# Performance work log

Measured on AMD Instinct MI355X. Metric: run time of the kernel, lower is better.

Reference implementation:

```python
import jax, jax.numpy as jnp
import numpy as np

TEMP = 5.0      # torch_kmeans SoftKMeans default temperature
N_ITERS = 25    # fixed iteration count (tolerance-based stop removed for jit)
EPS = 1e-9


def _soft_kmeans(x, l, key):
    # x: (r, q, d) -> labels (r, q) int32, centers (r, l, d)
    r, q, d = x.shape
    keys = jax.random.split(key, r)
    # random-point init (one permutation per batch, first l points)
    idx = jax.vmap(lambda k: jax.random.permutation(k, q)[:l])(keys)  # (r, l)
    centers = jnp.take_along_axis(x, idx[:, :, None], axis=1)         # (r, l, d)
    x_sq = jnp.sum(x * x, axis=-1)                                    # (r, q)

    def dist_to(centers):
        # squared euclidean distance (r, q, l)
        return (x_sq[:, :, None]
                - 2.0 * jnp.einsum('rqd,rld->rql', x, centers)
                + jnp.sum(centers * centers, axis=-1)[:, None, :])

    def step(centers, _):
        w = jax.nn.softmax(-TEMP * dist_to(centers), axis=-1)         # (r, q, l)
        denom = jnp.sum(w, axis=1)[:, :, None] + EPS                  # (r, l, 1)
        centers = jnp.einsum('rql,rqd->rld', w, x) / denom
        return centers, None

    centers, _ = jax.lax.scan(step, centers, None, length=N_ITERS)
    labels = jnp.argmin(dist_to(centers), axis=-1)                    # (r, q)
    return labels, centers


def setup_inputs() -> dict:
    key = jax.random.key(0)
    x = jax.random.normal(key, (8, 2048, 1024), dtype=jnp.float32)
    return {"x": x, "q": 4096, "r": 8, "l": 256}


def reference(x, q, r, l):
    B, T, F = x.shape
    # B*T*F must equal r*q*d; mirrors x.view(B,-1).view(B,q,-1).view(r,q,-1)
    xr = x.reshape(r, q, -1)
    labels, centers = _soft_kmeans(xr, l, jax.random.key(42))
    # gather centroid per point: rec[b, i, :] = centers[b, labels[b, i], :]
    rec = jnp.take_along_axis(centers, labels[:, :, None], axis=1)    # (r, q, d)
    return rec.reshape(B, T, F)
```

## Files before the change

kernel.cpp:

```cpp
#include <hip/hip_runtime.h>
#include <stdint.h>

#define RB 8
#define QN 4096
#define DN 512
#define LN 256
#define NITERS 25

typedef double f64x4 __attribute__((ext_vector_type(4)));

__device__ __forceinline__ void tf2x32(uint32_t k0, uint32_t k1,
                                       uint32_t x0, uint32_t x1,
                                       uint32_t& y0, uint32_t& y1) {
  uint32_t ks2 = k0 ^ k1 ^ 0x1BD11BDAu;
#define TFR(r) { x0 += x1; x1 = (x1 << (r)) | (x1 >> (32 - (r))); x1 ^= x0; }
  x0 += k0; x1 += k1;
  TFR(13) TFR(15) TFR(26) TFR(6)   x0 += k1;  x1 += ks2 + 1u;
  TFR(17) TFR(29) TFR(16) TFR(24)  x0 += ks2; x1 += k0 + 2u;
  TFR(13) TFR(15) TFR(26) TFR(6)   x0 += k0;  x1 += k1 + 3u;
  TFR(17) TFR(29) TFR(16) TFR(24)  x0 += k1;  x1 += ks2 + 4u;
  TFR(13) TFR(15) TFR(26) TFR(6)   x0 += ks2; x1 += k0 + 5u;
#undef TFR
  y0 = x0; y1 = x1;
}

__global__ __launch_bounds__(1024) void k_init(const float* __restrict__ x,
                                               float* __restrict__ centers) {
  __shared__ unsigned long long comp[QN];
  __shared__ unsigned short perm[QN];
  __shared__ unsigned short ptmp[QN];
  const int b = blockIdx.x, t = threadIdx.x;

  uint32_t kb0, kb1;
  tf2x32(0u, 42u, 0u, (uint32_t)b, kb0, kb1);

  for (int i = t; i < QN; i += 1024) perm[i] = (unsigned short)i;
  __syncthreads();

  for (int round = 0; round < 2; ++round) {
    uint32_t nk0, nk1, sk0, sk1;
    tf2x32(kb0, kb1, 0u, 0u, nk0, nk1);
    tf2x32(kb0, kb1, 0u, 1u, sk0, sk1);
    kb0 = nk0; kb1 = nk1;
    for (int i = t; i < QN; i += 1024) {
      uint32_t y0, y1;
      tf2x32(sk0, sk1, 0u, (uint32_t)i, y0, y1);
      uint32_t bits = y0 ^ y1;
      comp[i] = ((unsigned long long)bits << 32) | (unsigned)i;
    }
    __syncthreads();
    for (int k = 2; k <= QN; k <<= 1) {
      for (int j = k >> 1; j > 0; j >>= 1) {
        for (int i = t; i < QN; i += 1024) {
          int ixj = i ^ j;
          if (ixj > i) {
            unsigned long long vi = comp[i], vj = comp[ixj];
            bool up = ((i & k) == 0);
            bool sw = up ? (vi > vj) : (vi < vj);
            if (sw) { comp[i] = vj; comp[ixj] = vi; }
          }
        }
        __syncthreads();
      }
    }
    for (int i = t; i < QN; i += 1024) ptmp[i] = perm[(unsigned)(comp[i] & 0xFFFFu)];
    __syncthreads();
    for (int i = t; i < QN; i += 1024) perm[i] = ptmp[i];
    __syncthreads();
  }

  const float4* xb = (const float4*)(x + (size_t)b * QN * DN);
  float4* cb = (float4*)(centers + (size_t)b * LN * DN);
  for (int e = t; e < LN * (DN / 4); e += 1024) {
    int row = e >> 7;
    int c = e & 127;
    cb[(size_t)row * 128 + c] = xb[(size_t)perm[row] * 128 + c];
  }
}

__global__ __launch_bounds__(256) void k_rowsq_d(const float* __restrict__ a,
                                                 double* __restrict__ o, int nrows) {
  int w = (blockIdx.x * 256 + threadIdx.x) >> 6;
  int lane = threadIdx.x & 63;
  if (w >= nrows) return;
  const float* row = a + (size_t)w * DN;
  double s = 0.0;
  for (int i = lane; i < DN; i += 64) { double v = (double)row[i]; s = fma(v, v, s); }
#pragma unroll
  for (int off = 32; off; off >>= 1) s += __shfl_down(s, off);
  if (lane == 0) o[w] = s;
}

__global__ __launch_bounds__(64) void k_probe(int* __restrict__ flag) {
  __shared__ double xT[16][17];
  __shared__ double cT[16][17];
  const int t = threadIdx.x;
  for (int i = t; i < 256; i += 64) {
    int r = i >> 4, d = i & 15;
    xT[d][r] = (double)(r * 5 + d * 3 + 1);
    cT[d][r] = (double)(r * 2 + d * 7 + 2);
  }
  __syncthreads();
  const int kg = t >> 4, li = t & 15;
  f64x4 acc = {0.0, 0.0, 0.0, 0.0};
#pragma unroll
  for (int kk = 0; kk < 4; kk++) {
    double a  = xT[kk * 4 + kg][li];
    double bv = cT[kk * 4 + kg][li];
    acc = __builtin_amdgcn_mfma_f64_16x16x4f64(a, bv, acc, 0, 0, 0);
  }
  bool ok1 = true, ok2 = true;
#pragma unroll
  for (int d = 0; d < 4; d++) {
    int q1 = kg * 4 + d;
    int q2 = kg + 4 * d;
    double ref1 = 0.0, ref2 = 0.0;
    for (int dd = 0; dd < 16; dd++) {
      ref1 += xT[dd][q1] * cT[dd][li];
      ref2 += xT[dd][q2] * cT[dd][li];
    }
    ok1 = ok1 && (acc[d] == ref1);
    ok2 = ok2 && (acc[d] == ref2);
  }
  unsigned long long v1 = __ballot(ok1);
  unsigned long long v2 = __ballot(ok2);
  if (t == 0) *flag = (v1 == ~0ull) ? 1 : ((v2 == ~0ull) ? 2 : 0);
}

#define QT 64
#define XPD 68
#define CPD 260

__global__ __launch_bounds__(256, 2) void k_assign_mfma(const float* __restrict__ x,
                                                        const float* __restrict__ centers,
                                                        const double* __restrict__ csqd,
                                                        float* __restrict__ W,
                                                        const int* __restrict__ flag) {
  const int mode = *flag;
  if (mode == 0) return;
  __shared__ double xT[16][XPD];
  __shared__ double cT[16][CPD];
  const int b = blockIdx.y, q0 = blockIdx.x * QT, t = threadIdx.x;
  const int w = t >> 6, lane = t & 63;
  const int kg = lane >> 4, li = lane & 15;

  f64x4 acc[16];
#pragma unroll
  for (int i = 0; i < 16; i++) acc[i] = (f64x4){0.0, 0.0, 0.0, 0.0};

  const float* xb = x + ((size_t)b * QN + q0) * DN;
  const float* cb = centers + (size_t)b * LN * DN;
  const int xrow = t >> 2, xc4 = t & 3;

  float4 gx, gc[4];
  gx = *(const float4*)(xb + (size_t)xrow * DN + xc4 * 4);
#pragma unroll
  for (int i = 0; i < 4; i++) {
    int f = t + 256 * i; int row = f >> 2, c4 = f & 3;
    gc[i] = *(const float4*)(cb + (size_t)row * DN + c4 * 4);
  }

  for (int d0 = 0; d0 < DN; d0 += 16) {
    xT[xc4 * 4 + 0][xrow] = (double)gx.x;
    xT[xc4 * 4 + 1][xrow] = (double)gx.y;
    xT[xc4 * 4 + 2][xrow] = (double)gx.z;
    xT[xc4 * 4 + 3][xrow] = (double)gx.w;
#pragma unroll
    for (int i = 0; i < 4; i++) {
      int f = t + 256 * i; int row = f >> 2, c4 = f & 3;
      cT[c4 * 4 + 0][row] = (double)gc[i].x;
      cT[c4 * 4 + 1][row] = (double)gc[i].y;
      cT[c4 * 4 + 2][row] = (double)gc[i].z;
      cT[c4 * 4 + 3][row] = (double)gc[i].w;
    }
    __syncthreads();
    if (d0 + 16 < DN) {
      gx = *(const float4*)(xb + (size_t)xrow * DN + (d0 + 16) + xc4 * 4);
#pragma unroll
      for (int i = 0; i < 4; i++) {
        int f = t + 256 * i; int row = f >> 2, c4 = f & 3;
        gc[i] = *(const float4*)(cb + (size_t)row * DN + (d0 + 16) + c4 * 4);
      }
    }
#pragma unroll
    for (int kk = 0; kk < 4; kk++) {
      double a = xT[kk * 4 + kg][w * 16 + li];
#pragma unroll
      for (int t16 = 0; t16 < 16; t16++) {
        double bv = cT[kk * 4 + kg][t16 * 16 + li];
        acc[t16] = __builtin_amdgcn_mfma_f64_16x16x4f64(a, bv, acc[t16], 0, 0, 0);
      }
    }
    __syncthreads();
  }

  double m[4] = {-1e300, -1e300, -1e300, -1e300};
#pragma unroll
  for (int t16 = 0; t16 < 16; t16++) {
    double cq = csqd[b * LN + t16 * 16 + li];
#pragma unroll
    for (int d = 0; d < 4; d++) {
      double lg = -5.0 * (cq - 2.0 * acc[t16][d]);
      acc[t16][d] = lg;
      m[d] = fmax(m[d], lg);
    }
  }
#pragma unroll
  for (int off = 1; off < 16; off <<= 1)
#pragma unroll
    for (int d = 0; d < 4; d++) m[d] = fmax(m[d], __shfl_xor(m[d], off, 64));

  double s[4] = {0.0, 0.0, 0.0, 0.0};
#pragma unroll
  for (int t16 = 0; t16 < 16; t16++)
#pragma unroll
    for (int d = 0; d < 4; d++) {
      double e = exp(acc[t16][d] - m[d]);
      acc[t16][d] = e;
      s[d] += e;
    }
#pragma unroll
  for (int off = 1; off < 16; off <<= 1)
#pragma unroll
    for (int d = 0; d < 4; d++) s[d] += __shfl_xor(s[d], off, 64);

  const size_t qbase = (size_t)b * QN + q0 + w * 16;
#pragma unroll
  for (int d = 0; d < 4; d++) {
    int qrow = (mode == 1) ? (kg * 4 + d) : (kg + 4 * d);
    float* wrow = W + (qbase + qrow) * LN + li;
    double inv = 1.0 / s[d];
#pragma unroll
    for (int t16 = 0; t16 < 16; t16++)
      wrow[t16 * 16] = (float)(acc[t16][d] * inv);
  }
}

#define DK 16
#define XLD 82
#define CLDf 260
__device__ __forceinline__ int grow(int q) { return q + ((q >> 3) << 1); }

__global__ __launch_bounds__(256, 2) void k_assign_valu(const float* __restrict__ x,
                                                        const float* __restrict__ centers,
                                                        const double* __restrict__ csqd,
                                                        float* __restrict__ W,
                                                        const int* __restrict__ flag) {
  if (*flag != 0) return;
  __shared__ double xsD[DK][XLD];
  __shared__ float  csF[DK][CLDf];
  __shared__ double red[QT][33];
  const int b = blockIdx.y, q0 = blockIdx.x * QT, t = threadIdx.x;
  const int rg = t & 7, cg = t >> 3;
  double acc[8][8];
#pragma unroll
  for (int i = 0; i < 8; i++)
#pragma unroll
    for (int j = 0; j < 8; j++) acc[i][j] = 0.0;

  const float* xb = x + ((size_t)b * QN + q0) * DN;
  const float* cb = centers + (size_t)b * LN * DN;
  const int xrow = t >> 2, xc4 = t & 3;
  const int xg = grow(xrow);

  float4 gx, gc[4];
  gx = *(const float4*)(xb + (size_t)xrow * DN + xc4 * 4);
#pragma unroll
  for (int i = 0; i < 4; i++) {
    int f = t + 256 * i; int row = f >> 2, c4 = f & 3;
    gc[i] = *(const float4*)(cb + (size_t)row * DN + c4 * 4);
  }

  for (int d0 = 0; d0 < DN; d0 += DK) {
    xsD[xc4 * 4 + 0][xg] = (double)gx.x; xsD[xc4 * 4 + 1][xg] = (double)gx.y;
    xsD[xc4 * 4 + 2][xg] = (double)gx.z; xsD[xc4 * 4 + 3][xg] = (double)gx.w;
#pragma unroll
    for (int i = 0; i < 4; i++) {
      int f = t + 256 * i; int row = f >> 2, c4 = f & 3;
      csF[c4 * 4 + 0][row] = gc[i].x; csF[c4 * 4 + 1][row] = gc[i].y;
      csF[c4 * 4 + 2][row] = gc[i].z; csF[c4 * 4 + 3][row] = gc[i].w;
    }
    __syncthreads();
    if (d0 + DK < DN) {
      gx = *(const float4*)(xb + (size_t)xrow * DN + (d0 + DK) + xc4 * 4);
#pragma unroll
      for (int i = 0; i < 4; i++) {
        int f = t + 256 * i; int row = f >> 2, c4 = f & 3;
        gc[i] = *(const float4*)(cb + (size_t)row * DN + (d0 + DK) + c4 * 4);
      }
    }
    double xva[8]; float4 ca0, ca1;
#pragma unroll
    for (int j = 0; j < 8; j++) xva[j] = xsD[0][rg * 10 + j];
    ca0 = *(const float4*)&csF[0][cg * 8];
    ca1 = *(const float4*)&csF[0][cg * 8 + 4];
#pragma unroll
    for (int k = 0; k < DK; k++) {
      double xvb[8]; float4 cb0, cb1;
      if (k + 1 < DK) {
#pragma unroll
        for (int j = 0; j < 8; j++) xvb[j] = xsD[k + 1][rg * 10 + j];
        cb0 = *(const float4*)&csF[k + 1][cg * 8];
        cb1 = *(const float4*)&csF[k + 1][cg * 8 + 4];
      }
      double cv[8] = {(double)ca0.x, (double)ca0.y, (double)ca0.z, (double)ca0.w,
                      (double)ca1.x, (double)ca1.y, (double)ca1.z, (double)ca1.w};
#pragma unroll
      for (int i = 0; i < 8; i++)
#pragma unroll
        for (int j = 0; j < 8; j++)
          acc[i][j] = fma(xva[i], cv[j], acc[i][j]);
      if (k + 1 < DK) {
#pragma unroll
        for (int j = 0; j < 8; j++) xva[j] = xvb[j];
        ca0 = cb0; ca1 = cb1;
      }
    }
    __syncthreads();
  }

  double csqv[8];
#pragma unroll
  for (int j = 0; j < 8; j++) csqv[j] = csqd[b * LN + cg * 8 + j];

  double lmax[8];
#pragma unroll
  for (int i = 0; i < 8; i++) {
    double m = -1e300;
#pragma unroll
    for (int j = 0; j < 8; j++) {
      double lg = -5.0 * (csqv[j] - 2.0 * acc[i][j]);
      acc[i][j] = lg;
      m = fmax(m, lg);
    }
    lmax[i] = m;
  }
#pragma unroll
  for (int i = 0; i < 8; i++) red[rg * 8 + i][cg] = lmax[i];
  __syncthreads();
  double rmax[8];
#pragma unroll
  for (int i = 0; i < 8; i++) {
    double m = -1e300;
    for (int c = 0; c < 32; c++) m = fmax(m, red[rg * 8 + i][c]);
    rmax[i] = m;
  }
  __syncthreads();
#pragma unroll
  for (int i = 0; i < 8; i++) {
    double s = 0.0;
#pragma unroll
    for (int j = 0; j < 8; j++) {
      double e = exp(acc[i][j] - rmax[i]);
      acc[i][j] = e;
      s += e;
    }
    red[rg * 8 + i][cg] = s;
  }
  __syncthreads();
#pragma unroll
  for (int i = 0; i < 8; i++) {
    double s = 0.0;
    for (int c = 0; c < 32; c++) s += red[rg * 8 + i][c];
    float* wrow = W + ((size_t)b * QN + q0 + rg * 8 + i) * LN + cg * 8;
    float4 v0 = make_float4((float)(acc[i][0] / s), (float)(acc[i][1] / s),
                            (float)(acc[i][2] / s), (float)(acc[i][3] / s));
    float4 v1 = make_float4((float)(acc[i][4] / s), (float)(acc[i][5] / s),
                            (float)(acc[i][6] / s), (float)(acc[i][7] / s));
    *(float4*)wrow = v0;
    *(float4*)(wrow + 4) = v1;
  }
}

#define NCH 8
#define CHQ (QN / NCH)
#define UKQ 16

__global__ __launch_bounds__(256, 3) void k_update_split(
    const float* __restrict__ W, const float* __restrict__ x,
    float* __restrict__ P, float* __restrict__ dsum) {
  __shared__ float wT[UKQ][132];
  __shared__ float xT[UKQ][132];
  const int b = blockIdx.z;
  const int s = blockIdx.y;
  const int lt = (blockIdx.x >> 2) * 128;
  const int dt = (blockIdx.x & 3) * 128;
  const int t = threadIdx.x;
  const int tr = t >> 4, tc = t & 15;
  float acc[8][8];
#pragma unroll
  for (int i = 0; i < 8; i++)
#pragma unroll
    for (int j = 0; j < 8; j++) acc[i][j] = 0.f;
  float dsm[8] = {0, 0, 0, 0, 0, 0, 0, 0};

  const float* Wb = W + ((size_t)b * QN + (size_t)s * CHQ) * LN + lt;
  const float* xb = x + ((size_t)b * QN + (size_t)s * CHQ) * DN + dt;

  float4 gw[2], gx2[2];
#pragma unroll
  for (int i = 0; i < 2; i++) {
    int f = t + 256 * i; int row = f >> 5, c = f & 31;
    gw[i]  = *(const float4*)(Wb + (size_t)row * LN + c * 4);
    gx2[i] = *(const float4*)(xb + (size_t)row * DN + c * 4);
  }

  for (int k0 = 0; k0 < CHQ; k0 += UKQ) {
#pragma unroll
    for (int i = 0; i < 2; i++) {
      int f = t + 256 * i; int row = f >> 5, c = f & 31;
      *(float4*)&wT[row][c * 4] = gw[i];
      *(float4*)&xT[row][c * 4] = gx2[i];
    }
    __syncthreads();
    if (k0 + UKQ < CHQ) {
#pragma unroll
      for (int i = 0; i < 2; i++) {
        int f = t + 256 * i; int row = f >> 5, c = f & 31;
        gw[i]  = *(const float4*)(Wb + (size_t)(k0 + UKQ + row) * LN + c * 4);
        gx2[i] = *(const float4*)(xb + (size_t)(k0 + UKQ + row) * DN + c * 4);
      }
    }
#pragma unroll
    for (int k = 0; k < UKQ; k++) {
      float4 w0 = *(const float4*)&wT[k][tr * 4];
      float4 w1 = *(const float4*)&wT[k][64 + tr * 4];
      float4 x0 = *(const float4*)&xT[k][tc * 4];
      float4 x1 = *(const float4*)&xT[k][64 + tc * 4];
      float wf[8] = {w0.x, w0.y, w0.z, w0.w, w1.x, w1.y, w1.z, w1.w};
      float xf[8] = {x0.x, x0.y, x0.z, x0.w, x1.x, x1.y, x1.z, x1.w};
#pragma unroll
      for (int i = 0; i < 8; i++) {
        dsm[i] += wf[i];
#pragma unroll
        for (int j = 0; j < 8; j++) acc[i][j] = fmaf(wf[i], xf[j], acc[i][j]);
      }
    }
    __syncthreads();
  }

#pragma unroll
  for (int i = 0; i < 8; i++) {
    int l = lt + ((i < 4) ? (tr * 4 + i) : (64 + tr * 4 + i - 4));
    float* prow = P + (((size_t)s * RB + b) * LN + l) * DN + dt;
    *(float4*)(prow + tc * 4)      = make_float4(acc[i][0], acc[i][1], acc[i][2], acc[i][3]);
    *(float4*)(prow + 64 + tc * 4) = make_float4(acc[i][4], acc[i][5], acc[i][6], acc[i][7]);
    if (tc == 0) dsum[((size_t)s * RB + b) * LN + l] = dsm[i];
  }
}

__global__ __launch_bounds__(128) void k_reduce(const float* __restrict__ P,
                                                const float* __restrict__ dsum,
                                                float* __restrict__ cnew,
                                                double* __restrict__ csqd) {
  const int row = blockIdx.x;
  const int b = row >> 8, l = row & 255;
  const int t = threadIdx.x;
  float dn = 0.f;
#pragma unroll
  for (int s = 0; s < NCH; s++) dn += dsum[((size_t)s * RB + b) * LN + l];
  float den = dn + 1e-9f;
  float4 v = make_float4(0.f, 0.f, 0.f, 0.f);
#pragma unroll
  for (int s = 0; s < NCH; s++) {
    float4 p = *(const float4*)(P + (((size_t)s * RB + b) * LN + l) * DN + t * 4);
    v.x += p.x; v.y += p.y; v.z += p.z; v.w += p.w;
  }
  float4 o = make_float4(v.x / den, v.y / den, v.z / den, v.w / den);
  *(float4*)(cnew + ((size_t)b * LN + l) * DN + t * 4) = o;
  double sq = (double)o.x * o.x + (double)o.y * o.y +
              (double)o.z * o.z + (double)o.w * o.w;
#pragma unroll
  for (int off = 32; off; off >>= 1) sq += __shfl_down(sq, off);
  __shared__ double sred[2];
  if ((t & 63) == 0) sred[t >> 6] = sq;
  __syncthreads();
  if (t == 0) csqd[row] = sred[0] + sred[1];
}

#define LT 64
#define DT 64
#define KQ 32
__global__ __launch_bounds__(256) void k_update_mono(const float* __restrict__ W,
                                                     const float* __restrict__ x,
                                                     float* __restrict__ cnew) {
  __shared__ float wT[KQ][LT + 4];
  __shared__ float xT[KQ][DT + 4];
  const int b = blockIdx.z;
  const int l0 = blockIdx.x * LT;
  const int d0 = blockIdx.y * DT;
  const int t = threadIdx.x;
  const int rg = t & 15;
  const int cg = t >> 4;
  float acc[4][4];
#pragma unroll
  for (int i = 0; i < 4; i++)
#pragma unroll
    for (int j = 0; j < 4; j++) acc[i][j] = 0.f;
  float dsm[4] = {0.f, 0.f, 0.f, 0.f};
  const float* Wb = W + (size_t)b * QN * LN;
  const float* xb = x + (size_t)b * QN * DN;
  for (int k0 = 0; k0 < QN; k0 += KQ) {
#pragma unroll
    for (int i = 0; i < 2; i++) {
      int f = t + 256 * i;
      int row = f >> 4, c4 = f & 15;
      *(float4*)&wT[row][c4 * 4] = *(const float4*)(Wb + (size_t)(k0 + row) * LN + l0 + c4 * 4);
    }
#pragma unroll
    for (int i = 0; i < 2; i++) {
      int f = t + 256 * i;
      int row = f >> 4, c4 = f & 15;
      *(float4*)&xT[row][c4 * 4] = *(const float4*)(xb + (size_t)(k0 + row) * DN + d0 + c4 * 4);
    }
    __syncthreads();
#pragma unroll
    for (int k = 0; k < KQ; k++) {
      float wf[4], xf[4];
      *(float4*)wf = *(const float4*)&wT[k][rg * 4];
      *(float4*)xf = *(const float4*)&xT[k][cg * 4];
#pragma unroll
      for (int i = 0; i < 4; i++) {
        dsm[i] += wf[i];
#pragma unroll
        for (int j = 0; j < 4; j++) acc[i][j] = fmaf(wf[i], xf[j], acc[i][j]);
      }
    }
    __syncthreads();
  }
#pragma unroll
  for (int i = 0; i < 4; i++) {
    float den = dsm[i] + 1e-9f;
    *(float4*)(cnew + ((size_t)b * LN + l0 + rg * 4 + i) * DN + d0 + cg * 4) =
        make_float4(acc[i][0] / den, acc[i][1] / den, acc[i][2] / den, acc[i][3] / den);
  }
}

__global__ __launch_bounds__(256, 2) void k_final(const float* __restrict__ x,
                                                  const float* __restrict__ centers,
                                                  const double* __restrict__ csqd,
                                                  float* __restrict__ out) {
  __shared__ double xsD[DK][XLD];
  __shared__ float  csF[DK][CLDf];
  __shared__ double redv[QT][33];
  __shared__ unsigned short redi[QT][33];
  __shared__ unsigned short labels[QT];
  const int b = blockIdx.y, q0 = blockIdx.x * QT, t = threadIdx.x;
  const int rg = t & 7, cg = t >> 3;
  double acc[8][8];
#pragma unroll
  for (int i = 0; i < 8; i++)
#pragma unroll
    for (int j = 0; j < 8; j++) acc[i][j] = 0.0;

  const float* xb = x + ((size_t)b * QN + q0) * DN;
  const float* cb = centers + (size_t)b * LN * DN;
  const int xrow = t >> 2, xc4 = t & 3;
  const int xg = grow(xrow);

  float4 gx, gc[4];
  gx = *(const float4*)(xb + (size_t)xrow * DN + xc4 * 4);
#pragma unroll
  for (int i = 0; i < 4; i++) {
    int f = t + 256 * i; int row = f >> 2, c4 = f & 3;
    gc[i] = *(const float4*)(cb + (size_t)row * DN + c4 * 4);
  }

  for (int d0 = 0; d0 < DN; d0 += DK) {
    xsD[xc4 * 4 + 0][xg] = (double)gx.x; xsD[xc4 * 4 + 1][xg] = (double)gx.y;
    xsD[xc4 * 4 + 2][xg] = (double)gx.z; xsD[xc4 * 4 + 3][xg] = (double)gx.w;
#pragma unroll
    for (int i = 0; i < 4; i++) {
      int f = t + 256 * i; int row = f >> 2, c4 = f & 3;
      csF[c4 * 4 + 0][row] = gc[i].x; csF[c4 * 4 + 1][row] = gc[i].y;
      csF[c4 * 4 + 2][row] = gc[i].z; csF[c4 * 4 + 3][row] = gc[i].w;
    }
    __syncthreads();
    if (d0 + DK < DN) {
      gx = *(const float4*)(xb + (size_t)xrow * DN + (d0 + DK) + xc4 * 4);
#pragma unroll
      for (int i = 0; i < 4; i++) {
        int f = t + 256 * i; int row = f >> 2, c4 = f & 3;
        gc[i] = *(const float4*)(cb + (size_t)row * DN + (d0 + DK) + c4 * 4);
      }
    }
    double xva[8]; float4 ca0, ca1;
#pragma unroll
    for (int j = 0; j < 8; j++) xva[j] = xsD[0][rg * 10 + j];
    ca0 = *(const float4*)&csF[0][cg * 8];
    ca1 = *(const float4*)&csF[0][cg * 8 + 4];
#pragma unroll
    for (int k = 0; k < DK; k++) {
      double xvb[8]; float4 cb0, cb1;
      if (k + 1 < DK) {
#pragma unroll
        for (int j = 0; j < 8; j++) xvb[j] = xsD[k + 1][rg * 10 + j];
        cb0 = *(const float4*)&csF[k + 1][cg * 8];
        cb1 = *(const float4*)&csF[k + 1][cg * 8 + 4];
      }
      double cv[8] = {(double)ca0.x, (double)ca0.y, (double)ca0.z, (double)ca0.w,
                      (double)ca1.x, (double)ca1.y, (double)ca1.z, (double)ca1.w};
#pragma unroll
      for (int i = 0; i < 8; i++)
#pragma unroll
        for (int j = 0; j < 8; j++)
          acc[i][j] = fma(xva[i], cv[j], acc[i][j]);
      if (k + 1 < DK) {
#pragma unroll
        for (int j = 0; j < 8; j++) xva[j] = xvb[j];
        ca0 = cb0; ca1 = cb1;
      }
    }
    __syncthreads();
  }

  double csqv[8];
#pragma unroll
  for (int j = 0; j < 8; j++) csqv[j] = csqd[b * LN + cg * 8 + j];

  double bv[8]; int bi[8];
#pragma unroll
  for (int i = 0; i < 8; i++) {
    bv[i] = 1e300; bi[i] = 0;
#pragma unroll
    for (int j = 0; j < 8; j++) {
      double dd = csqv[j] - 2.0 * acc[i][j];
      if (dd < bv[i]) { bv[i] = dd; bi[i] = cg * 8 + j; }
    }
  }
#pragma unroll
  for (int i = 0; i < 8; i++) {
    redv[rg * 8 + i][cg] = bv[i];
    redi[rg * 8 + i][cg] = (unsigned short)bi[i];
  }
  __syncthreads();
  if (t < QT) {
    double best = 1e300; int bidx = 0;
    for (int c = 0; c < 32; c++) {
      double v = redv[t][c];
      int id = redi[t][c];
      if (v < best || (v == best && id < bidx)) { best = v; bidx = id; }
    }
    labels[t] = (unsigned short)bidx;
  }
  __syncthreads();
  const float4* cb4 = (const float4*)(centers + (size_t)b * LN * DN);
  float4* ob = (float4*)(out + ((size_t)b * QN + q0) * DN);
  for (int e = t; e < QT * (DN / 4); e += 256) {
    int row = e >> 7, c = e & 127;
    ob[(size_t)row * 128 + c] = cb4[(size_t)labels[row] * 128 + c];
  }
}

extern "C" void kernel_launch(void* const* d_in, const int* in_sizes, int n_in,
                              void* d_out, int out_size, void* d_ws, size_t ws_size,
                              hipStream_t stream) {
  const float* x = (const float*)d_in[0];
  float* out = (float*)d_out;

  const size_t szC    = (size_t)RB * LN * DN * sizeof(float);
  const size_t szCsqD = (size_t)RB * LN * sizeof(double);
  const size_t szDsum = (size_t)NCH * RB * LN * sizeof(float);
  const size_t szFlag = 256;
  const size_t szW    = (size_t)RB * QN * LN * sizeof(float);

  char* p = (char*)d_ws;
  float*  cA   = (float*)p;  p += szC;
  float*  cB   = (float*)p;  p += szC;
  double* csqd = (double*)p; p += szCsqD;
  float*  dsum = (float*)p;  p += szDsum;
  int*    flag = (int*)p;    p += szFlag;
  const bool bigws = ws_size >= 2 * szC + szCsqD + szDsum + szFlag + szW;
  float* W = bigws ? (float*)p : (float*)d_out;
  float* P = (float*)d_out;

  k_probe<<<1, 64, 0, stream>>>(flag);
  k_init<<<RB, 1024, 0, stream>>>(x, cA);
  k_rowsq_d<<<(RB * LN) / 4, 256, 0, stream>>>(cA, csqd, RB * LN);

  float* cur = cA;
  float* nxt = cB;
  for (int it = 0; it < NITERS; ++it) {
    k_assign_mfma<<<dim3(QN / QT, RB), 256, 0, stream>>>(x, cur, csqd, W, flag);
    k_assign_valu<<<dim3(QN / QT, RB), 256, 0, stream>>>(x, cur, csqd, W, flag);
    if (bigws) {
      k_update_split<<<dim3(8, NCH, RB), 256, 0, stream>>>(W, x, P, dsum);
      k_reduce<<<RB * LN, 128, 0, stream>>>(P, dsum, nxt, csqd);
    } else {
      k_update_mono<<<dim3(LN / LT, DN / DT, RB), 256, 0, stream>>>(W, x, nxt);
      k_rowsq_d<<<(RB * LN) / 4, 256, 0, stream>>>(nxt, csqd, RB * LN);
    }
    float* tmp = cur; cur = nxt; nxt = tmp;
  }
  k_final<<<dim3(QN / QT, RB), 256, 0, stream>>>(x, cur, csqd, out);
}
```

Measured before the change: 7.803 ms.

## Merge assign kernels and retile FP64 MFMA as 4x4 tiles per wave

The separate MFMA and VALU assignment kernels become one kernel that branches on the probe flag, so each iteration launches one kernel instead of two. The MFMA path is retiled: each wave now owns a 64-query by 64-center block built from 4x4 MFMA tiles, reusing four A and four B fragments across 16 MFMAs instead of reloading B for every MFMA. Because a wave now covers only part of the centers, the softmax max and sum need a cross-wave reduction through shared memory, which adds two extra barriers. Both paths share one shared-memory arena sized for the larger of the two.

Measured after the change: 8.011 ms. 2.7% more time.

```diff
diff --git a/kernel.cpp b/kernel.cpp
--- a/kernel.cpp
+++ b/kernel.cpp
@@ -130,245 +130,287 @@
 #define QT 64
 #define XPD 68
 #define CPD 260
-
-__global__ __launch_bounds__(256, 2) void k_assign_mfma(const float* __restrict__ x,
-                                                        const float* __restrict__ centers,
-                                                        const double* __restrict__ csqd,
-                                                        float* __restrict__ W,
-                                                        const int* __restrict__ flag) {
-  const int mode = *flag;
-  if (mode == 0) return;
-  __shared__ double xT[16][XPD];
-  __shared__ double cT[16][CPD];
-  const int b = blockIdx.y, q0 = blockIdx.x * QT, t = threadIdx.x;
-  const int w = t >> 6, lane = t & 63;
-  const int kg = lane >> 4, li = lane & 15;
-
-  f64x4 acc[16];
-#pragma unroll
-  for (int i = 0; i < 16; i++) acc[i] = (f64x4){0.0, 0.0, 0.0, 0.0};
-
-  const float* xb = x + ((size_t)b * QN + q0) * DN;
-  const float* cb = centers + (size_t)b * LN * DN;
-  const int xrow = t >> 2, xc4 = t & 3;
-
-  float4 gx, gc[4];
-  gx = *(const float4*)(xb + (size_t)xrow * DN + xc4 * 4);
-#pragma unroll
-  for (int i = 0; i < 4; i++) {
-    int f = t + 256 * i; int row = f >> 2, c4 = f & 3;
-    gc[i] = *(const float4*)(cb + (size_t)row * DN + c4 * 4);
-  }
-
-  for (int d0 = 0; d0 < DN; d0 += 16) {
-    xT[xc4 * 4 + 0][xrow] = (double)gx.x;
-    xT[xc4 * 4 + 1][xrow] = (double)gx.y;
-    xT[xc4 * 4 + 2][xrow] = (double)gx.z;
-    xT[xc4 * 4 + 3][xrow] = (double)gx.w;
-#pragma unroll
-    for (int i = 0; i < 4; i++) {
-      int f = t + 256 * i; int row = f >> 2, c4 = f & 3;
-      cT[c4 * 4 + 0][row] = (double)gc[i].x;
-      cT[c4 * 4 + 1][row] = (double)gc[i].y;
-      cT[c4 * 4 + 2][row] = (double)gc[i].z;
-      cT[c4 * 4 + 3][row] = (double)gc[i].w;
-    }
-    __syncthreads();
-    if (d0 + 16 < DN) {
-      gx = *(const float4*)(xb + (size_t)xrow * DN + (d0 + 16) + xc4 * 4);
-#pragma unroll
-      for (int i = 0; i < 4; i++) {
-        int f = t + 256 * i; int row = f >> 2, c4 = f & 3;
-        gc[i] = *(const float4*)(cb + (size_t)row * DN + (d0 + 16) + c4 * 4);
-      }
-    }
-#pragma unroll
-    for (int kk = 0; kk < 4; kk++) {
-      double a = xT[kk * 4 + kg][w * 16 + li];
-#pragma unroll
-      for (int t16 = 0; t16 < 16; t16++) {
-        double bv = cT[kk * 4 + kg][t16 * 16 + li];
-        acc[t16] = __builtin_amdgcn_mfma_f64_16x16x4f64(a, bv, acc[t16], 0, 0, 0);
-      }
-    }
-    __syncthreads();
-  }
-
-  double m[4] = {-1e300, -1e300, -1e300, -1e300};
-#pragma unroll
-  for (int t16 = 0; t16 < 16; t16++) {
-    double cq = csqd[b * LN + t16 * 16 + li];
-#pragma unroll
-    for (int d = 0; d < 4; d++) {
-      double lg = -5.0 * (cq - 2.0 * acc[t16][d]);
-      acc[t16][d] = lg;
-      m[d] = fmax(m[d], lg);
-    }
-  }
-#pragma unroll
-  for (int off = 1; off < 16; off <<= 1)
-#pragma unroll
-    for (int d = 0; d < 4; d++) m[d] = fmax(m[d], __shfl_xor(m[d], off, 64));
-
-  double s[4] = {0.0, 0.0, 0.0, 0.0};
-#pragma unroll
-  for (int t16 = 0; t16 < 16; t16++)
-#pragma unroll
-    for (int d = 0; d < 4; d++) {
-      double e = exp(acc[t16][d] - m[d]);
-      acc[t16][d] = e;
-      s[d] += e;
-    }
-#pragma unroll
-  for (int off = 1; off < 16; off <<= 1)
-#pragma unroll
-    for (int d = 0; d < 4; d++) s[d] += __shfl_xor(s[d], off, 64);
-
-  const size_t qbase = (size_t)b * QN + q0 + w * 16;
-#pragma unroll
-  for (int d = 0; d < 4; d++) {
-    int qrow = (mode == 1) ? (kg * 4 + d) : (kg + 4 * d);
-    float* wrow = W + (qbase + qrow) * LN + li;
-    double inv = 1.0 / s[d];
-#pragma unroll
-    for (int t16 = 0; t16 < 16; t16++)
-      wrow[t16 * 16] = (float)(acc[t16][d] * inv);
-  }
-}
-
 #define DK 16
 #define XLD 82
 #define CLDf 260
 __device__ __forceinline__ int grow(int q) { return q + ((q >> 3) << 1); }
 
-__global__ __launch_bounds__(256, 2) void k_assign_valu(const float* __restrict__ x,
-                                                        const float* __restrict__ centers,
-                                                        const double* __restrict__ csqd,
-                                                        float* __restrict__ W,
-                                                        const int* __restrict__ flag) {
-  if (*flag != 0) return;
-  __shared__ double xsD[DK][XLD];
-  __shared__ float  csF[DK][CLDf];
-  __shared__ double red[QT][33];
+#define ARENA_D 5888
+
+__global__ __launch_bounds__(256, 2) void k_assign(const float* __restrict__ x,
+                                                   const float* __restrict__ centers,
+                                                   const double* __restrict__ csqd,
+                                                   float* __restrict__ W,
+                                                   const int* __restrict__ flag) {
+  __shared__ double arena[ARENA_D];
+  const int mode = *flag;
   const int b = blockIdx.y, q0 = blockIdx.x * QT, t = threadIdx.x;
-  const int rg = t & 7, cg = t >> 3;
-  double acc[8][8];
-#pragma unroll
-  for (int i = 0; i < 8; i++)
-#pragma unroll
-    for (int j = 0; j < 8; j++) acc[i][j] = 0.0;
-
   const float* xb = x + ((size_t)b * QN + q0) * DN;
   const float* cb = centers + (size_t)b * LN * DN;
   const int xrow = t >> 2, xc4 = t & 3;
-  const int xg = grow(xrow);
-
-  float4 gx, gc[4];
-  gx = *(const float4*)(xb + (size_t)xrow * DN + xc4 * 4);
-#pragma unroll
-  for (int i = 0; i < 4; i++) {
-    int f = t + 256 * i; int row = f >> 2, c4 = f & 3;
-    gc[i] = *(const float4*)(cb + (size_t)row * DN + c4 * 4);
-  }
-
-  for (int d0 = 0; d0 < DN; d0 += DK) {
-    xsD[xc4 * 4 + 0][xg] = (double)gx.x; xsD[xc4 * 4 + 1][xg] = (double)gx.y;
-    xsD[xc4 * 4 + 2][xg] = (double)gx.z; xsD[xc4 * 4 + 3][xg] = (double)gx.w;
+
+  if (mode != 0) {
+    double (*xT)[XPD]  = (double(*)[XPD])arena;
+    double (*cT)[CPD]  = (double(*)[CPD])(arena + 16 * XPD);
+    double (*redm)[5]  = (double(*)[5])(arena + 16 * XPD + 16 * CPD);
+    double (*reds)[5]  = (double(*)[5])(arena + 16 * XPD + 16 * CPD + 320);
+    const int w = t >> 6, lane = t & 63;
+    const int kg = lane >> 4, li = lane & 15;
+
+    f64x4 acc[4][4];
+#pragma unroll
+    for (int i = 0; i < 4; i++)
+#pragma unroll
+      for (int j = 0; j < 4; j++) acc[i][j] = (f64x4){0.0, 0.0, 0.0, 0.0};
+
+    float4 gx, gc[4];
+    gx = *(const float4*)(xb + (size_t)xrow * DN + xc4 * 4);
 #pragma unroll
     for (int i = 0; i < 4; i++) {
       int f = t + 256 * i; int row = f >> 2, c4 = f & 3;
-      csF[c4 * 4 + 0][row] = gc[i].x; csF[c4 * 4 + 1][row] = gc[i].y;
-      csF[c4 * 4 + 2][row] = gc[i].z; csF[c4 * 4 + 3][row] = gc[i].w;
-    }
-    __syncthreads();
-    if (d0 + DK < DN) {
-      gx = *(const float4*)(xb + (size_t)xrow * DN + (d0 + DK) + xc4 * 4);
+      gc[i] = *(const float4*)(cb + (size_t)row * DN + c4 * 4);
+    }
+
+    for (int d0 = 0; d0 < DN; d0 += 16) {
+      xT[xc4 * 4 + 0][xrow] = (double)gx.x;
+      xT[xc4 * 4 + 1][xrow] = (double)gx.y;
+      xT[xc4 * 4 + 2][xrow] = (double)gx.z;
+      xT[xc4 * 4 + 3][xrow] = (double)gx.w;
 #pragma unroll
       for (int i = 0; i < 4; i++) {
         int f = t + 256 * i; int row = f >> 2, c4 = f & 3;
-        gc[i] = *(const float4*)(cb + (size_t)row * DN + (d0 + DK) + c4 * 4);
-      }
-    }
-    double xva[8]; float4 ca0, ca1;
-#pragma unroll
-    for (int j = 0; j < 8; j++) xva[j] = xsD[0][rg * 10 + j];
-    ca0 = *(const float4*)&csF[0][cg * 8];
-    ca1 = *(const float4*)&csF[0][cg * 8 + 4];
-#pragma unroll
-    for (int k = 0; k < DK; k++) {
-      double xvb[8]; float4 cb0, cb1;
-      if (k + 1 < DK) {
-#pragma unroll
-        for (int j = 0; j < 8; j++) xvb[j] = xsD[k + 1][rg * 10 + j];
-        cb0 = *(const float4*)&csF[k + 1][cg * 8];
-        cb1 = *(const float4*)&csF[k + 1][cg * 8 + 4];
-      }
-      double cv[8] = {(double)ca0.x, (double)ca0.y, (double)ca0.z, (double)ca0.w,
-                      (double)ca1.x, (double)ca1.y, (double)ca1.z, (double)ca1.w};
-#pragma unroll
-      for (int i = 0; i < 8; i++)
-#pragma unroll
-        for (int j = 0; j < 8; j++)
-          acc[i][j] = fma(xva[i], cv[j], acc[i][j]);
-      if (k + 1 < DK) {
-#pragma unroll
-        for (int j = 0; j < 8; j++) xva[j] = xvb[j];
-        ca0 = cb0; ca1 = cb1;
-      }
-    }
-    __syncthreads();
-  }
-
-  double csqv[8];
-#pragma unroll
-  for (int j = 0; j < 8; j++) csqv[j] = csqd[b * LN + cg * 8 + j];
-
-  double lmax[8];
-#pragma unroll
-  for (int i = 0; i < 8; i++) {
-    double m = -1e300;
-#pragma unroll
-    for (int j = 0; j < 8; j++) {
-      double lg = -5.0 * (csqv[j] - 2.0 * acc[i][j]);
-      acc[i][j] = lg;
-      m = fmax(m, lg);
-    }
-    lmax[i] = m;
-  }
-#pragma unroll
-  for (int i = 0; i < 8; i++) red[rg * 8 + i][cg] = lmax[i];
-  __syncthreads();
-  double rmax[8];
-#pragma unroll
-  for (int i = 0; i < 8; i++) {
-    double m = -1e300;
-    for (int c = 0; c < 32; c++) m = fmax(m, red[rg * 8 + i][c]);
-    rmax[i] = m;
-  }
-  __syncthreads();
-#pragma unroll
-  for (int i = 0; i < 8; i++) {
-    double s = 0.0;
-#pragma unroll
-    for (int j = 0; j < 8; j++) {
-      double e = exp(acc[i][j] - rmax[i]);
-      acc[i][j] = e;
-      s += e;
-    }
-    red[rg * 8 + i][cg] = s;
-  }
-  __syncthreads();
-#pragma unroll
-  for (int i = 0; i < 8; i++) {
-    double s = 0.0;
-    for (int c = 0; c < 32; c++) s += red[rg * 8 + i][c];
-    float* wrow = W + ((size_t)b * QN + q0 + rg * 8 + i) * LN + cg * 8;
-    float4 v0 = make_float4((float)(acc[i][0] / s), (float)(acc[i][1] / s),
-                            (float)(acc[i][2] / s), (float)(acc[i][3] / s));
-    float4 v1 = make_float4((float)(acc[i][4] / s), (float)(acc[i][5] / s),
-                            (float)(acc[i][6] / s), (float)(acc[i][7] / s));
-    *(float4*)wrow = v0;
-    *(float4*)(wrow + 4) = v1;
+        cT[c4 * 4 + 0][row] = (double)gc[i].x;
+        cT[c4 * 4 + 1][row] = (double)gc[i].y;
+        cT[c4 * 4 + 2][row] = (double)gc[i].z;
+        cT[c4 * 4 + 3][row] = (double)gc[i].w;
+      }
+      __syncthreads();
+      if (d0 + 16 < DN) {
+        gx = *(const float4*)(xb + (size_t)xrow * DN + (d0 + 16) + xc4 * 4);
+#pragma unroll
+        for (int i = 0; i < 4; i++) {
+          int f = t + 256 * i; int row = f >> 2, c4 = f & 3;
+          gc[i] = *(const float4*)(cb + (size_t)row * DN + (d0 + 16) + c4 * 4);
+        }
+      }
+#pragma unroll
+      for (int kk = 0; kk < 4; kk++) {
+        double a[4], bf[4];
+#pragma unroll
+        for (int qt = 0; qt < 4; qt++) a[qt] = xT[kk * 4 + kg][qt * 16 + li];
+#pragma unroll
+        for (int lt = 0; lt < 4; lt++) bf[lt] = cT[kk * 4 + kg][w * 64 + lt * 16 + li];
+#pragma unroll
+        for (int qt = 0; qt < 4; qt++)
+#pragma unroll
+          for (int lt = 0; lt < 4; lt++)
+            acc[qt][lt] = __builtin_amdgcn_mfma_f64_16x16x4f64(a[qt], bf[lt], acc[qt][lt], 0, 0, 0);
+      }
+      __syncthreads();
+    }
+
+    double csqv[4];
+#pragma unroll
+    for (int lt = 0; lt < 4; lt++) csqv[lt] = csqd[b * LN + w * 64 + lt * 16 + li];
+
+    double rm[4][4];
+#pragma unroll
+    for (int qt = 0; qt < 4; qt++)
+#pragma unroll
+      for (int d = 0; d < 4; d++) {
+        double m = -1e300;
+#pragma unroll
+        for (int lt = 0; lt < 4; lt++) {
+          double lg = -5.0 * (csqv[lt] - 2.0 * acc[qt][lt][d]);
+          acc[qt][lt][d] = lg;
+          m = fmax(m, lg);
+        }
+        rm[qt][d] = m;
+      }
+#pragma unroll
+    for (int off = 1; off < 16; off <<= 1)
+#pragma unroll
+      for (int qt = 0; qt < 4; qt++)
+#pragma unroll
+        for (int d = 0; d < 4; d++) rm[qt][d] = fmax(rm[qt][d], __shfl_xor(rm[qt][d], off, 64));
+    if (li == 0) {
+#pragma unroll
+      for (int qt = 0; qt < 4; qt++)
+#pragma unroll
+        for (int d = 0; d < 4; d++) {
+          int qr = qt * 16 + ((mode == 1) ? (kg * 4 + d) : (kg + 4 * d));
+          redm[qr][w] = rm[qt][d];
+        }
+    }
+    __syncthreads();
+#pragma unroll
+    for (int qt = 0; qt < 4; qt++)
+#pragma unroll
+      for (int d = 0; d < 4; d++) {
+        int qr = qt * 16 + ((mode == 1) ? (kg * 4 + d) : (kg + 4 * d));
+        rm[qt][d] = fmax(fmax(redm[qr][0], redm[qr][1]), fmax(redm[qr][2], redm[qr][3]));
+      }
+    double sv[4][4];
+#pragma unroll
+    for (int qt = 0; qt < 4; qt++)
+#pragma unroll
+      for (int d = 0; d < 4; d++) {
+        double s = 0.0;
+#pragma unroll
+        for (int lt = 0; lt < 4; lt++) {
+          double e = exp(acc[qt][lt][d] - rm[qt][d]);
+          acc[qt][lt][d] = e;
+          s += e;
+        }
+        sv[qt][d] = s;
+      }
+#pragma unroll
+    for (int off = 1; off < 16; off <<= 1)
+#pragma unroll
+      for (int qt = 0; qt < 4; qt++)
+#pragma unroll
+        for (int d = 0; d < 4; d++) sv[qt][d] += __shfl_xor(sv[qt][d], off, 64);
+    if (li == 0) {
+#pragma unroll
+      for (int qt = 0; qt < 4; qt++)
+#pragma unroll
+        for (int d = 0; d < 4; d++) {
+          int qr = qt * 16 + ((mode == 1) ? (kg * 4 + d) : (kg + 4 * d));
+          reds[qr][w] = sv[qt][d];
+        }
+    }
+    __syncthreads();
+#pragma unroll
+    for (int qt = 0; qt < 4; qt++)
+#pragma unroll
+      for (int d = 0; d < 4; d++) {
+        int qr = qt * 16 + ((mode == 1) ? (kg * 4 + d) : (kg + 4 * d));
+        double tot = reds[qr][0] + reds[qr][1] + reds[qr][2] + reds[qr][3];
+        double inv = 1.0 / tot;
+        float* wr = W + ((size_t)b * QN + q0 + qr) * LN + w * 64 + li;
+#pragma unroll
+        for (int lt = 0; lt < 4; lt++)
+          wr[lt * 16] = (float)(acc[qt][lt][d] * inv);
+      }
+  } else {
+    double (*xsD)[XLD]  = (double(*)[XLD])arena;
+    float  (*csF)[CLDf] = (float(*)[CLDf])(arena + 16 * XLD);
+    double (*red)[33]   = (double(*)[33])(arena + 16 * XLD + (16 * CLDf) / 2);
+    const int rg = t & 7, cg = t >> 3;
+    double acc[8][8];
+#pragma unroll
+    for (int i = 0; i < 8; i++)
+#pragma unroll
+      for (int j = 0; j < 8; j++) acc[i][j] = 0.0;
+
+    const int xg = grow(xrow);
+    float4 gx, gc[4];
+    gx = *(const float4*)(xb + (size_t)xrow * DN + xc4 * 4);
+#pragma unroll
+    for (int i = 0; i < 4; i++) {
+      int f = t + 256 * i; int row = f >> 2, c4 = f & 3;
+      gc[i] = *(const float4*)(cb + (size_t)row * DN + c4 * 4);
+    }
+
+    for (int d0 = 0; d0 < DN; d0 += DK) {
+      xsD[xc4 * 4 + 0][xg] = (double)gx.x; xsD[xc4 * 4 + 1][xg] = (double)gx.y;
+      xsD[xc4 * 4 + 2][xg] = (double)gx.z; xsD[xc4 * 4 + 3][xg] = (double)gx.w;
+#pragma unroll
+      for (int i = 0; i < 4; i++) {
+        int f = t + 256 * i; int row = f >> 2, c4 = f & 3;
+        csF[c4 * 4 + 0][row] = gc[i].x; csF[c4 * 4 + 1][row] = gc[i].y;
+        csF[c4 * 4 + 2][row] = gc[i].z; csF[c4 * 4 + 3][row] = gc[i].w;
+      }
+      __syncthreads();
+      if (d0 + DK < DN) {
+        gx = *(const float4*)(xb + (size_t)xrow * DN + (d0 + DK) + xc4 * 4);
+#pragma unroll
+        for (int i = 0; i < 4; i++) {
+          int f = t + 256 * i; int row = f >> 2, c4 = f & 3;
+          gc[i] = *(const float4*)(cb + (size_t)row * DN + (d0 + DK) + c4 * 4);
+        }
+      }
+      double xva[8]; float4 ca0, ca1;
+#pragma unroll
+      for (int j = 0; j < 8; j++) xva[j] = xsD[0][rg * 10 + j];
+      ca0 = *(const float4*)&csF[0][cg * 8];
+      ca1 = *(const float4*)&csF[0][cg * 8 + 4];
+#pragma unroll
+      for (int k = 0; k < DK; k++) {
+        double xvb[8]; float4 cb0, cb1;
+        if (k + 1 < DK) {
+#pragma unroll
+          for (int j = 0; j < 8; j++) xvb[j] = xsD[k + 1][rg * 10 + j];
+          cb0 = *(const float4*)&csF[k + 1][cg * 8];
+          cb1 = *(const float4*)&csF[k + 1][cg * 8 + 4];
+        }
+        double cv[8] = {(double)ca0.x, (double)ca0.y, (double)ca0.z, (double)ca0.w,
+                        (double)ca1.x, (double)ca1.y, (double)ca1.z, (double)ca1.w};
+#pragma unroll
+        for (int i = 0; i < 8; i++)
+#pragma unroll
+          for (int j = 0; j < 8; j++)
+            acc[i][j] = fma(xva[i], cv[j], acc[i][j]);
+        if (k + 1 < DK) {
+#pragma unroll
+          for (int j = 0; j < 8; j++) xva[j] = xvb[j];
+          ca0 = cb0; ca1 = cb1;
+        }
+      }
+      __syncthreads();
+    }
+
+    double csqv[8];
+#pragma unroll
+    for (int j = 0; j < 8; j++) csqv[j] = csqd[b * LN + cg * 8 + j];
+
+    double lmax[8];
+#pragma unroll
+    for (int i = 0; i < 8; i++) {
+      double m = -1e300;
+#pragma unroll
+      for (int j = 0; j < 8; j++) {
+        double lg = -5.0 * (csqv[j] - 2.0 * acc[i][j]);
+        acc[i][j] = lg;
+        m = fmax(m, lg);
+      }
+      lmax[i] = m;
+    }
+#pragma unroll
+    for (int i = 0; i < 8; i++) red[rg * 8 + i][cg] = lmax[i];
+    __syncthreads();
+    double rmax[8];
+#pragma unroll
+    for (int i = 0; i < 8; i++) {
+      double m = -1e300;
+      for (int c = 0; c < 32; c++) m = fmax(m, red[rg * 8 + i][c]);
+      rmax[i] = m;
+    }
+    __syncthreads();
+#pragma unroll
+    for (int i = 0; i < 8; i++) {
+      double s = 0.0;
+#pragma unroll
+      for (int j = 0; j < 8; j++) {
+        double e = exp(acc[i][j] - rmax[i]);
+        acc[i][j] = e;
+        s += e;
+      }
+      red[rg * 8 + i][cg] = s;
+    }
+    __syncthreads();
+#pragma unroll
+    for (int i = 0; i < 8; i++) {
+      double s = 0.0;
+      for (int c = 0; c < 32; c++) s += red[rg * 8 + i][c];
+      float* wrow = W + ((size_t)b * QN + q0 + rg * 8 + i) * LN + cg * 8;
+      float4 v0 = make_float4((float)(acc[i][0] / s), (float)(acc[i][1] / s),
+                              (float)(acc[i][2] / s), (float)(acc[i][3] / s));
+      float4 v1 = make_float4((float)(acc[i][4] / s), (float)(acc[i][5] / s),
+                              (float)(acc[i][6] / s), (float)(acc[i][7] / s));
+      *(float4*)wrow = v0;
+      *(float4*)(wrow + 4) = v1;
+    }
   }
 }
 
@@ -681,8 +723,7 @@
   float* cur = cA;
   float* nxt = cB;
   for (int it = 0; it < NITERS; ++it) {
-    k_assign_mfma<<<dim3(QN / QT, RB), 256, 0, stream>>>(x, cur, csqd, W, flag);
-    k_assign_valu<<<dim3(QN / QT, RB), 256, 0, stream>>>(x, cur, csqd, W, flag);
+    k_assign<<<dim3(QN / QT, RB), 256, 0, stream>>>(x, cur, csqd, W, flag);
     if (bigws) {
       k_update_split<<<dim3(8, NCH, RB), 256, 0, stream>>>(W, x, P, dsum);
       k_reduce<<<RB * LN, 128, 0, stream>>>(P, dsum, nxt, csqd);
```
